# Kernel tuning notes

Measured on AMD Instinct MI355X. Metric: run time of the kernel, lower is better.

## Reference

```python
import jax, jax.numpy as jnp
import numpy as np

EMBED = 1024
HEADS = 16
HEAD_DIM = EMBED // HEADS          # 64
EXP_DIM = 2 * HEAD_DIM             # 128


def setup_inputs() -> dict:
    key = jax.random.key(0)
    ks = jax.random.split(key, 7)
    N, S = 4, 2048
    values = jax.random.normal(ks[0], (N, S, EMBED), dtype=jnp.float32)
    keys_ = jax.random.normal(ks[1], (N, S, EMBED), dtype=jnp.float32)
    query = jax.random.normal(ks[2], (N, S, EMBED), dtype=jnp.float32)
    # feature map linear: initialized to identity weight, zero bias (per init_weights),
    # perturb slightly so it's a nontrivial learned map
    fm_w = jnp.eye(HEAD_DIM, dtype=jnp.float32) + 0.02 * jax.random.normal(ks[3], (HEAD_DIM, HEAD_DIM), dtype=jnp.float32)
    fm_b = 0.02 * jax.random.normal(ks[4], (HEAD_DIM,), dtype=jnp.float32)
    fc_w = jax.random.normal(ks[5], (EMBED, HEADS * EXP_DIM), dtype=jnp.float32) * (1.0 / np.sqrt(HEADS * EXP_DIM))
    fc_b = jnp.zeros((EMBED,), dtype=jnp.float32)
    return {"values": values, "keys": keys_, "query": query,
            "fm_w": fm_w, "fm_b": fm_b, "fc_w": fc_w, "fc_b": fc_b}


def _feature_map(x, fm_w, fm_b):
    # x: [n, s, h, d] -> [n, s, h, 2d]
    z = jnp.einsum('nshd,ed->nshe', x, fm_w) + fm_b
    return jnp.concatenate([jnp.exp(z), jnp.exp(-z)], axis=-1)


def reference(values, keys, query, fm_w, fm_b, fc_w, fc_b):
    N, S, _ = query.shape
    v = values.reshape(N, -1, HEADS, HEAD_DIM)
    k = keys.reshape(N, -1, HEADS, HEAD_DIM)
    q = query.reshape(N, -1, HEADS, HEAD_DIM)
    v, k, q = (_feature_map(x, fm_w, fm_b) for x in (v, k, q))  # [n,s,h,2d]
    scores = jnp.einsum('nqhd,nkhd->nhqk', q, k) / jnp.sqrt(jnp.float32(EMBED))
    attn = jax.nn.softmax(scores, axis=-1)
    out = jnp.einsum('nhql,nlhd->nqhd', attn, v)  # [n,q,h,2d]
    out = out.reshape(N, S, HEADS * EXP_DIM)
    return out @ fc_w.T + fc_b
```

## Files before the change

### kernel.cpp

```cpp
#include <hip/hip_runtime.h>
#include <hip/hip_bf16.h>
#include <stdint.h>

#define N_B 4
#define SEQ 2048
#define NH 16
#define ED 128
#define EMB 1024
#define FCK 2048

typedef float f32x4 __attribute__((ext_vector_type(4)));
typedef float f32x16 __attribute__((ext_vector_type(16)));
typedef _Float16 f16x8 __attribute__((ext_vector_type(8)));
typedef _Float16 f16x4 __attribute__((ext_vector_type(4)));
typedef __fp16 fp16v2 __attribute__((ext_vector_type(2)));

__device__ __forceinline__ void gload16(const void* g, void* l) {
    __builtin_amdgcn_global_load_lds(
        (const __attribute__((address_space(1))) uint32_t*)(g),
        (__attribute__((address_space(3))) uint32_t*)(l), 16, 0, 0);
}

__device__ __forceinline__ int pk2(float a, float b) {
    union { fp16v2 h; int i; } u;
    u.h = __builtin_amdgcn_cvt_pkrtz(a, b);
    return u.i;
}

__device__ __forceinline__ f16x8 frag4(int d0, int d1, int d2, int d3) {
    union { int i[4]; f16x8 v; } u;
    u.i[0] = d0; u.i[1] = d1; u.i[2] = d2; u.i[3] = d3;
    return u.v;
}

__global__ __launch_bounds__(256) void fmap_kernel(
    const float* __restrict__ vals, const float* __restrict__ keys,
    const float* __restrict__ qry,  const float* __restrict__ fmw,
    const float* __restrict__ fmb,
    _Float16* __restrict__ qf, _Float16* __restrict__ kf,
    _Float16* __restrict__ vf)
{
    const int lane = threadIdx.x & 63;
    const int w = threadIdx.x >> 6;
    const int t = blockIdx.x * 4 + w;
    const int n = t >> 11;
    const int s = t & 2047;
    const int r = lane & 15;
    const int g = lane >> 4;

    f16x8 whf[4][2], wlf[4][2];
    #pragma unroll
    for (int te = 0; te < 4; ++te) {
      #pragma unroll
      for (int j = 0; j < 2; ++j) {
        const float* p = fmw + (te*16 + r)*64 + j*32 + 8*g;
        #pragma unroll
        for (int i = 0; i < 8; ++i) {
            float wv = p[i];
            _Float16 hi = (_Float16)wv;
            whf[te][j][i] = hi;
            wlf[te][j][i] = (_Float16)(wv - (float)hi);
        }
      }
    }
    float bias[4];
    #pragma unroll
    for (int te = 0; te < 4; ++te) bias[te] = fmb[te*16 + r];

    const float QSCL = 0.03125f * 1.4426950408889634f;

    const long rowoff = ((long)t*16 + r) * 64;
    const float* srcs[3] = {qry, keys, vals};
    #pragma unroll
    for (int tens = 0; tens < 3; ++tens) {
        const float* src = srcs[tens] + rowoff;
        f16x8 ah[2], al[2];
        #pragma unroll
        for (int j = 0; j < 2; ++j) {
            #pragma unroll
            for (int i = 0; i < 8; ++i) {
                float x = src[j*32 + 8*g + i];
                _Float16 hi = (_Float16)x;
                ah[j][i] = hi;
                al[j][i] = (_Float16)(x - (float)hi);
            }
        }
        #pragma unroll
        for (int te = 0; te < 4; ++te) {
            f32x4 c = (f32x4){0.f,0.f,0.f,0.f};
            c = __builtin_amdgcn_mfma_f32_16x16x32_f16(ah[0], whf[te][0], c, 0, 0, 0);
            c = __builtin_amdgcn_mfma_f32_16x16x32_f16(ah[1], whf[te][1], c, 0, 0, 0);
            c = __builtin_amdgcn_mfma_f32_16x16x32_f16(ah[0], wlf[te][0], c, 0, 0, 0);
            c = __builtin_amdgcn_mfma_f32_16x16x32_f16(ah[1], wlf[te][1], c, 0, 0, 0);
            c = __builtin_amdgcn_mfma_f32_16x16x32_f16(al[0], whf[te][0], c, 0, 0, 0);
            c = __builtin_amdgcn_mfma_f32_16x16x32_f16(al[1], whf[te][1], c, 0, 0, 0);
            #pragma unroll
            for (int i = 0; i < 4; ++i) {
                float z = c[i] + bias[te];
                float ep = __expf(z), en = __expf(-z);
                int hh = 4*g + i;
                int e = te*16 + r;
                long base = (((long)n*NH + hh)*SEQ + s)*ED;
                if (tens == 0) {
                    qf[base + e]      = (_Float16)(ep * QSCL);
                    qf[base + 64 + e] = (_Float16)(en * QSCL);
                } else if (tens == 1) {
                    kf[base + e]      = (_Float16)ep;
                    kf[base + 64 + e] = (_Float16)en;
                } else {
                    vf[base + e]      = (_Float16)ep;
                    vf[base + 64 + e] = (_Float16)en;
                }
            }
        }
    }
}

__global__ __launch_bounds__(256) void vtrans_kernel(
    const _Float16* __restrict__ vf, _Float16* __restrict__ vt)
{
    __shared__ _Float16 tile[64][72];
    const int b = blockIdx.x;
    const int et = b & 1;
    const int st = (b >> 1) & 31;
    const int nh = b >> 6;
    const _Float16* src = vf + ((long)nh*SEQ + st*64)*ED + et*64;
    const int col4 = (threadIdx.x & 15) * 4;
    const int row0 = threadIdx.x >> 4;
    #pragma unroll
    for (int j = 0; j < 4; ++j) {
        int row = row0 + j*16;
        *(f16x4*)&tile[row][col4] = *(const f16x4*)(src + (long)row*ED + col4);
    }
    __syncthreads();
    _Float16* dst = vt + ((long)nh*ED + et*64)*SEQ + st*64;
    const int erow = threadIdx.x >> 2;
    const int sc0 = (threadIdx.x & 3) * 16;
    f16x8 o0, o1;
    #pragma unroll
    for (int i = 0; i < 8; ++i) o0[i] = tile[sc0 + i][erow];
    #pragma unroll
    for (int i = 0; i < 8; ++i) o1[i] = tile[sc0 + 8 + i][erow];
    *(f16x8*)(dst + (long)erow*SEQ + sc0) = o0;
    *(f16x8*)(dst + (long)erow*SEQ + sc0 + 8) = o1;
}

__global__ __launch_bounds__(256) void cvt_kernel(
    const float* __restrict__ src, _Float16* __restrict__ dst)
{
    long i = ((long)blockIdx.x*256 + threadIdx.x)*8;
    f16x8 o;
    #pragma unroll
    for (int j = 0; j < 8; ++j) o[j] = (_Float16)src[i + j];
    *(f16x8*)(dst + i) = o;
}

__global__ __launch_bounds__(512, 2) void attn_kernel(
    const _Float16* __restrict__ qf,
    const _Float16* __restrict__ kf,
    const _Float16* __restrict__ vt,
    _Float16* __restrict__ ob)
{
    __shared__ char smem[65536];
    const int lane = threadIdx.x & 63;
    const int w = threadIdx.x >> 6;
    const int orig = blockIdx.x;
    const int b = ((orig & 7) << 6) | (orig >> 3);
    const int nh = b >> 3;
    const int n = nh >> 4, h = nh & 15;
    const int qt = (b & 7)*8 + w;
    const int q32 = lane & 31;
    const int hl = lane >> 5;

    const _Float16* qb = qf + (long)nh*SEQ*ED;
    const char* kg = (const char*)(kf + (long)nh*SEQ*ED);
    const char* vg = (const char*)(vt + (long)nh*ED*SEQ);

    f16x8 qfr[8];
    #pragma unroll
    for (int j = 0; j < 8; ++j)
        qfr[j] = *(const f16x8*)(qb + (long)(qt*32 + q32)*ED + 16*j + 8*hl);

    auto stage = [&](int kt, int bsel) {
        char* Kl = smem + bsel*32768;
        char* Vl = Kl + 16384;
        const char* kts = kg + (long)kt*64*256;
        const char* vts = vg + (long)kt*64*2;
        #pragma unroll
        for (int i = 0; i < 2; ++i) {
            int row = w*8 + i*4 + (lane>>4);
            int c = (lane&15) ^ (row&15);
            gload16(kts + (long)row*256 + c*16, Kl + (w*8 + i*4)*256);
        }
        #pragma unroll
        for (int i = 0; i < 2; ++i) {
            int row = w*16 + i*8 + (lane>>3);
            int c = (lane&7) ^ (row&7);
            gload16(vts + (long)row*(SEQ*2) + c*16, Vl + (w*16 + i*8)*128);
        }
    };

    f32x16 acc[4];
    #pragma unroll
    for (int vv = 0; vv < 4; ++vv)
      #pragma unroll
      for (int i = 0; i < 16; ++i) acc[vv][i] = 0.f;
    float mrun = -1e30f, lrun = 0.f;

    stage(0, 0);
    __syncthreads();

    const int kswz = q32 & 15;
    const int vswz = q32 & 7;

    for (int kt = 0; kt < SEQ/64; ++kt) {
        const int cur = kt & 1;
        if (kt + 1 < SEQ/64) stage(kt + 1, cur ^ 1);
        const char* Kl = smem + cur*32768;
        const char* Vl = Kl + 16384;

        f32x16 s0, s1;
        #pragma unroll
        for (int i = 0; i < 16; ++i) { s0[i] = 0.f; s1[i] = 0.f; }
        #pragma unroll
        for (int j = 0; j < 8; ++j) {
            int off = (((hl + 2*j) & 15) ^ kswz) << 4;
            f16x8 k0 = *(const f16x8*)(Kl + q32*256 + off);
            f16x8 k1 = *(const f16x8*)(Kl + 8192 + q32*256 + off);
            __builtin_amdgcn_s_setprio(1);
            s0 = __builtin_amdgcn_mfma_f32_32x32x16_f16(k0, qfr[j], s0, 0, 0, 0);
            s1 = __builtin_amdgcn_mfma_f32_32x32x16_f16(k1, qfr[j], s1, 0, 0, 0);
            __builtin_amdgcn_s_setprio(0);
        }

        float mx = s0[0];
        #pragma unroll
        for (int i = 1; i < 16; ++i) mx = fmaxf(mx, s0[i]);
        #pragma unroll
        for (int i = 0; i < 16; ++i) mx = fmaxf(mx, s1[i]);
        mx = fmaxf(mx, __shfl_xor(mx, 32, 64));
        if (__any(mx > mrun + 11.0f)) {
            float mnew = fmaxf(mrun, mx);
            float corr = exp2f(mrun - mnew);
            lrun *= corr;
            #pragma unroll
            for (int vv = 0; vv < 4; ++vv)
                #pragma unroll
                for (int i = 0; i < 16; ++i) acc[vv][i] *= corr;
            mrun = mnew;
        }
        int wreg[2][8];
        float rsum = 0.f;
        #pragma unroll
        for (int kk = 0; kk < 2; ++kk) {
            float p[16];
            #pragma unroll
            for (int i = 0; i < 16; ++i) {
                float sv = (kk == 0) ? s0[i] : s1[i];
                p[i] = exp2f(sv - mrun);
                rsum += p[i];
            }
            #pragma unroll
            for (int tW = 0; tW < 8; ++tW)
                wreg[kk][tW] = pk2(p[2*tW], p[2*tW + 1]);
        }
        rsum += __shfl_xor(rsum, 32, 64);
        lrun += rsum;

        f16x8 pa[4];
        #pragma unroll
        for (int kk = 0; kk < 2; ++kk) {
            #pragma unroll
            for (int par = 0; par < 2; ++par) {
                int a0 = wreg[kk][par*4 + 0], b0 = wreg[kk][par*4 + 2];
                int a1 = wreg[kk][par*4 + 1], b1 = wreg[kk][par*4 + 3];
                auto r0 = __builtin_amdgcn_permlane32_swap(a0, b0, false, false);
                auto r1 = __builtin_amdgcn_permlane32_swap(a1, b1, false, false);
                pa[kk*2 + par] = frag4(r0[0], r1[0], r0[1], r1[1]);
            }
        }

        #pragma unroll
        for (int ks = 0; ks < 4; ++ks) {
            f16x8 vfr[4];
            #pragma unroll
            for (int vv = 0; vv < 4; ++vv) {
                int vrow = vv*32 + q32;
                vfr[vv] = *(const f16x8*)(Vl + vrow*128 + (((2*ks + hl) ^ vswz) << 4));
            }
            __builtin_amdgcn_s_setprio(1);
            #pragma unroll
            for (int vv = 0; vv < 4; ++vv)
                acc[vv] = __builtin_amdgcn_mfma_f32_32x32x16_f16(vfr[vv], pa[ks], acc[vv], 0, 0, 0);
            __builtin_amdgcn_s_setprio(0);
        }
        __syncthreads();
    }

    float inv = 1.0f / lrun;
    int q = qt*32 + q32;
    long base = ((long)n*SEQ + q)*FCK + h*ED;
    #pragma unroll
    for (int vv = 0; vv < 4; ++vv) {
        #pragma unroll
        for (int rg = 0; rg < 4; ++rg) {
            f16x4 o;
            #pragma unroll
            for (int i = 0; i < 4; ++i) o[i] = (_Float16)(acc[vv][rg*4 + i] * inv);
            *(f16x4*)(ob + base + vv*32 + 8*rg + 4*hl) = o;
        }
    }
}

__global__ __launch_bounds__(256) void fc_kernel(
    const _Float16* __restrict__ ob,
    const _Float16* __restrict__ wt,
    const float* __restrict__ fcb,
    float* __restrict__ out)
{
    __shared__ char smem[32768];
    const int lane = threadIdx.x & 63;
    const int w = threadIdx.x >> 6;
    const int wm = w >> 1, wn = w & 1;
    const int r = lane & 15, g = lane >> 4;

    const int orig = blockIdx.x;
    const int tile = ((orig & 7) << 6) | (orig >> 3);
    const int mt = tile >> 3;
    const int nt = tile & 7;

    const char* Ag = (const char*)(ob + (long)mt*128*FCK);
    const char* Bg = (const char*)(wt + (long)nt*128*FCK);

    auto stage = [&](int kt, int bsel) {
        char* As = smem + bsel*16384;
        char* Bs = As + 8192;
        #pragma unroll
        for (int rnd = 0; rnd < 2; ++rnd) {
            int row = rnd*64 + w*16 + (lane >> 2);
            int cs = (lane & 3) ^ ((row >> 1) & 3);
            gload16(Ag + (long)row*(FCK*2) + kt*64 + cs*16, As + rnd*4096 + w*1024);
            gload16(Bg + (long)row*(FCK*2) + kt*64 + cs*16, Bs + rnd*4096 + w*1024);
        }
    };

    f32x4 acc[4][4];
    #pragma unroll
    for (int u = 0; u < 4; ++u)
      #pragma unroll
      for (int v = 0; v < 4; ++v) acc[u][v] = (f32x4){0.f,0.f,0.f,0.f};

    stage(0, 0);
    __syncthreads();

    for (int kt = 0; kt < FCK/32; ++kt) {
        const int cur = kt & 1;
        if (kt + 1 < FCK/32) stage(kt + 1, cur ^ 1);
        const char* As = smem + cur*16384;
        const char* Bs = As + 8192;

        f16x8 afr[4], bfr[4];
        #pragma unroll
        for (int u = 0; u < 4; ++u) {
            int row = wm*64 + u*16 + r;
            afr[u] = *(const f16x8*)(As + row*64 + ((g ^ ((row >> 1) & 3)) << 4));
        }
        #pragma unroll
        for (int v = 0; v < 4; ++v) {
            int row = wn*64 + v*16 + r;
            bfr[v] = *(const f16x8*)(Bs + row*64 + ((g ^ ((row >> 1) & 3)) << 4));
        }
        __builtin_amdgcn_s_setprio(1);
        #pragma unroll
        for (int u = 0; u < 4; ++u)
          #pragma unroll
          for (int v = 0; v < 4; ++v)
            acc[u][v] = __builtin_amdgcn_mfma_f32_16x16x32_f16(afr[u], bfr[v], acc[u][v], 0, 0, 0);
        __builtin_amdgcn_s_setprio(0);
        __syncthreads();
    }

    #pragma unroll
    for (int u = 0; u < 4; ++u)
      #pragma unroll
      for (int v = 0; v < 4; ++v) {
        int col = nt*128 + wn*64 + v*16 + r;
        float bias = fcb[col];
        #pragma unroll
        for (int i = 0; i < 4; ++i) {
            int row = mt*128 + wm*64 + u*16 + 4*g + i;
            out[(long)row*EMB + col] = acc[u][v][i] + bias;
        }
      }
}

extern "C" void kernel_launch(void* const* d_in, const int* in_sizes, int n_in,
                              void* d_out, int out_size, void* d_ws, size_t ws_size,
                              hipStream_t stream) {
    const float* vals = (const float*)d_in[0];
    const float* keys = (const float*)d_in[1];
    const float* qry  = (const float*)d_in[2];
    const float* fmw  = (const float*)d_in[3];
    const float* fmb  = (const float*)d_in[4];
    const float* fcw  = (const float*)d_in[5];
    const float* fcb  = (const float*)d_in[6];
    char* ws = (char*)d_ws;
    const long SZ = 33554432L;
    _Float16* qf = (_Float16*)(ws);
    _Float16* kf = (_Float16*)(ws + SZ);
    _Float16* vf = (_Float16*)(ws + 2*SZ);
    _Float16* vt = (_Float16*)(ws + 3*SZ);
    _Float16* ob = (_Float16*)(ws + 4*SZ);
    _Float16* wt = (_Float16*)(ws + 5*SZ);
    float* out = (float*)d_out;

    fmap_kernel<<<dim3(2048), dim3(256), 0, stream>>>(vals, keys, qry, fmw, fmb, qf, kf, vf);
    vtrans_kernel<<<dim3(4096), dim3(256), 0, stream>>>(vf, vt);
    cvt_kernel<<<dim3(1024), dim3(256), 0, stream>>>(fcw, wt);
    attn_kernel<<<dim3(512), dim3(512), 0, stream>>>(qf, kf, vt, ob);
    fc_kernel<<<dim3(512), dim3(256), 0, stream>>>(ob, wt, fcb, out);
}
```

Before: 297.3 us.

## Double KV tile to 128 keys per stage with 128KB LDS and simplified staging

```diff
diff --git a/kernel.cpp b/kernel.cpp
--- a/kernel.cpp
+++ b/kernel.cpp
@@ -13,6 +13,7 @@
 typedef float f32x16 __attribute__((ext_vector_type(16)));
 typedef _Float16 f16x8 __attribute__((ext_vector_type(8)));
 typedef _Float16 f16x4 __attribute__((ext_vector_type(4)));
+typedef _Float16 f16x2 __attribute__((ext_vector_type(2)));
 typedef __fp16 fp16v2 __attribute__((ext_vector_type(2)));
 
 __device__ __forceinline__ void gload16(const void* g, void* l) {
@@ -27,11 +28,17 @@
     return u.i;
 }
 
+__device__ __forceinline__ f16x2 asf16x2(int v) {
+    union { int i; f16x2 h; } u; u.i = v; return u.h;
+}
+
 __device__ __forceinline__ f16x8 frag4(int d0, int d1, int d2, int d3) {
     union { int i[4]; f16x8 v; } u;
     u.i[0] = d0; u.i[1] = d1; u.i[2] = d2; u.i[3] = d3;
     return u.v;
 }
+
+#define M3(a,b,c) fmaxf(fmaxf((a),(b)),(c))
 
 __global__ __launch_bounds__(256) void fmap_kernel(
     const float* __restrict__ vals, const float* __restrict__ keys,
@@ -161,9 +168,10 @@
     const _Float16* __restrict__ vt,
     _Float16* __restrict__ ob)
 {
-    __shared__ char smem[65536];
-    const int lane = threadIdx.x & 63;
-    const int w = threadIdx.x >> 6;
+    __shared__ char smem[131072];
+    const int tid = threadIdx.x;
+    const int lane = tid & 63;
+    const int w = tid >> 6;
     const int orig = blockIdx.x;
     const int b = ((orig & 7) << 6) | (orig >> 3);
     const int nh = b >> 3;
@@ -181,23 +189,23 @@
     for (int j = 0; j < 8; ++j)
         qfr[j] = *(const f16x8*)(qb + (long)(qt*32 + q32)*ED + 16*j + 8*hl);
 
+    const int srow = tid >> 4;
+    const int sc   = (tid & 15) ^ (srow & 15);
+    const long koff = (long)srow*256  + sc*16;
+    const long voff = (long)srow*4096 + sc*16;
+    const int  ldst = tid*16;
+
     auto stage = [&](int kt, int bsel) {
-        char* Kl = smem + bsel*32768;
-        char* Vl = Kl + 16384;
-        const char* kts = kg + (long)kt*64*256;
-        const char* vts = vg + (long)kt*64*2;
-        #pragma unroll
-        for (int i = 0; i < 2; ++i) {
-            int row = w*8 + i*4 + (lane>>4);
-            int c = (lane&15) ^ (row&15);
-            gload16(kts + (long)row*256 + c*16, Kl + (w*8 + i*4)*256);
-        }
-        #pragma unroll
-        for (int i = 0; i < 2; ++i) {
-            int row = w*16 + i*8 + (lane>>3);
-            int c = (lane&7) ^ (row&7);
-            gload16(vts + (long)row*(SEQ*2) + c*16, Vl + (w*16 + i*8)*128);
-        }
+        char* Kl = smem + bsel*65536;
+        char* Vl = Kl + 32768;
+        const char* ksrc = kg + (long)kt*32768 + koff;
+        const char* vsrc = vg + (long)kt*256   + voff;
+        #pragma unroll
+        for (int i = 0; i < 4; ++i)
+            gload16(ksrc + i*8192, Kl + i*8192 + ldst);
+        #pragma unroll
+        for (int i = 0; i < 4; ++i)
+            gload16(vsrc + (long)i*131072, Vl + i*8192 + ldst);
     };
 
     f32x16 acc[4];
@@ -211,88 +219,95 @@
     __syncthreads();
 
     const int kswz = q32 & 15;
-    const int vswz = q32 & 7;
-
-    for (int kt = 0; kt < SEQ/64; ++kt) {
+
+    for (int kt = 0; kt < SEQ/128; ++kt) {
         const int cur = kt & 1;
-        if (kt + 1 < SEQ/64) stage(kt + 1, cur ^ 1);
-        const char* Kl = smem + cur*32768;
-        const char* Vl = Kl + 16384;
-
-        f32x16 s0, s1;
-        #pragma unroll
-        for (int i = 0; i < 16; ++i) { s0[i] = 0.f; s1[i] = 0.f; }
-        #pragma unroll
-        for (int j = 0; j < 8; ++j) {
-            int off = (((hl + 2*j) & 15) ^ kswz) << 4;
-            f16x8 k0 = *(const f16x8*)(Kl + q32*256 + off);
-            f16x8 k1 = *(const f16x8*)(Kl + 8192 + q32*256 + off);
+        if (kt + 1 < SEQ/128) stage(kt + 1, cur ^ 1);
+        const char* Kl = smem + cur*65536;
+        const char* Vl = Kl + 32768;
+
+        #pragma unroll
+        for (int p = 0; p < 2; ++p) {
+            f32x16 s0, s1;
+            #pragma unroll
+            for (int i = 0; i < 16; ++i) { s0[i] = 0.f; s1[i] = 0.f; }
+            const char* Kb = Kl + (p*64 + q32)*256;
             __builtin_amdgcn_s_setprio(1);
-            s0 = __builtin_amdgcn_mfma_f32_32x32x16_f16(k0, qfr[j], s0, 0, 0, 0);
-            s1 = __builtin_amdgcn_mfma_f32_32x32x16_f16(k1, qfr[j], s1, 0, 0, 0);
+            #pragma unroll
+            for (int j = 0; j < 8; ++j) {
+                int off = (((hl + 2*j) & 15) ^ kswz) << 4;
+                f16x8 k0 = *(const f16x8*)(Kb + off);
+                f16x8 k1 = *(const f16x8*)(Kb + 8192 + off);
+                s0 = __builtin_amdgcn_mfma_f32_32x32x16_f16(k0, qfr[j], s0, 0, 0, 0);
+                s1 = __builtin_amdgcn_mfma_f32_32x32x16_f16(k1, qfr[j], s1, 0, 0, 0);
+            }
             __builtin_amdgcn_s_setprio(0);
-        }
-
-        float mx = s0[0];
-        #pragma unroll
-        for (int i = 1; i < 16; ++i) mx = fmaxf(mx, s0[i]);
-        #pragma unroll
-        for (int i = 0; i < 16; ++i) mx = fmaxf(mx, s1[i]);
-        mx = fmaxf(mx, __shfl_xor(mx, 32, 64));
-        if (__any(mx > mrun + 11.0f)) {
-            float mnew = fmaxf(mrun, mx);
-            float corr = exp2f(mrun - mnew);
-            lrun *= corr;
-            #pragma unroll
-            for (int vv = 0; vv < 4; ++vv)
+
+            float mx = M3(s0[0], s0[1], s0[2]);
+            mx = M3(mx, s0[3], s0[4]);   mx = M3(mx, s0[5], s0[6]);
+            mx = M3(mx, s0[7], s0[8]);   mx = M3(mx, s0[9], s0[10]);
+            mx = M3(mx, s0[11], s0[12]); mx = M3(mx, s0[13], s0[14]);
+            mx = M3(mx, s0[15], s1[0]);  mx = M3(mx, s1[1], s1[2]);
+            mx = M3(mx, s1[3], s1[4]);   mx = M3(mx, s1[5], s1[6]);
+            mx = M3(mx, s1[7], s1[8]);   mx = M3(mx, s1[9], s1[10]);
+            mx = M3(mx, s1[11], s1[12]); mx = M3(mx, s1[13], s1[14]);
+            mx = fmaxf(mx, s1[15]);
+            mx = fmaxf(mx, __shfl_xor(mx, 32, 64));
+            if (__any(mx > mrun + 8.0f)) {
+                float mnew = fmaxf(mrun, mx);
+                float corr = exp2f(mrun - mnew);
+                lrun *= corr;
                 #pragma unroll
-                for (int i = 0; i < 16; ++i) acc[vv][i] *= corr;
-            mrun = mnew;
-        }
-        int wreg[2][8];
-        float rsum = 0.f;
-        #pragma unroll
-        for (int kk = 0; kk < 2; ++kk) {
-            float p[16];
-            #pragma unroll
-            for (int i = 0; i < 16; ++i) {
-                float sv = (kk == 0) ? s0[i] : s1[i];
-                p[i] = exp2f(sv - mrun);
-                rsum += p[i];
-            }
-            #pragma unroll
-            for (int tW = 0; tW < 8; ++tW)
-                wreg[kk][tW] = pk2(p[2*tW], p[2*tW + 1]);
-        }
-        rsum += __shfl_xor(rsum, 32, 64);
-        lrun += rsum;
-
-        f16x8 pa[4];
-        #pragma unroll
-        for (int kk = 0; kk < 2; ++kk) {
-            #pragma unroll
-            for (int par = 0; par < 2; ++par) {
-                int a0 = wreg[kk][par*4 + 0], b0 = wreg[kk][par*4 + 2];
-                int a1 = wreg[kk][par*4 + 1], b1 = wreg[kk][par*4 + 3];
-                auto r0 = __builtin_amdgcn_permlane32_swap(a0, b0, false, false);
-                auto r1 = __builtin_amdgcn_permlane32_swap(a1, b1, false, false);
-                pa[kk*2 + par] = frag4(r0[0], r1[0], r0[1], r1[1]);
-            }
-        }
-
-        #pragma unroll
-        for (int ks = 0; ks < 4; ++ks) {
-            f16x8 vfr[4];
-            #pragma unroll
-            for (int vv = 0; vv < 4; ++vv) {
-                int vrow = vv*32 + q32;
-                vfr[vv] = *(const f16x8*)(Vl + vrow*128 + (((2*ks + hl) ^ vswz) << 4));
-            }
-            __builtin_amdgcn_s_setprio(1);
-            #pragma unroll
-            for (int vv = 0; vv < 4; ++vv)
-                acc[vv] = __builtin_amdgcn_mfma_f32_32x32x16_f16(vfr[vv], pa[ks], acc[vv], 0, 0, 0);
-            __builtin_amdgcn_s_setprio(0);
+                for (int vv = 0; vv < 4; ++vv)
+                    #pragma unroll
+                    for (int i = 0; i < 16; ++i) acc[vv][i] *= corr;
+                mrun = mnew;
+            }
+            int wreg[2][8];
+            f16x2 psum = (f16x2){(_Float16)0.f, (_Float16)0.f};
+            #pragma unroll
+            for (int kk = 0; kk < 2; ++kk) {
+                #pragma unroll
+                for (int tW = 0; tW < 8; ++tW) {
+                    float sa = (kk == 0) ? s0[2*tW]   : s1[2*tW];
+                    float sb = (kk == 0) ? s0[2*tW+1] : s1[2*tW+1];
+                    int pw = pk2(exp2f(sa - mrun), exp2f(sb - mrun));
+                    wreg[kk][tW] = pw;
+                    psum += asf16x2(pw);
+                }
+            }
+            float rsum = (float)psum[0] + (float)psum[1];
+            rsum += __shfl_xor(rsum, 32, 64);
+            lrun += rsum;
+
+            f16x8 pa[4];
+            #pragma unroll
+            for (int kk = 0; kk < 2; ++kk) {
+                #pragma unroll
+                for (int par = 0; par < 2; ++par) {
+                    int a0 = wreg[kk][par*4 + 0], b0 = wreg[kk][par*4 + 2];
+                    int a1 = wreg[kk][par*4 + 1], b1 = wreg[kk][par*4 + 3];
+                    auto r0 = __builtin_amdgcn_permlane32_swap(a0, b0, false, false);
+                    auto r1 = __builtin_amdgcn_permlane32_swap(a1, b1, false, false);
+                    pa[kk*2 + par] = frag4(r0[0], r1[0], r0[1], r1[1]);
+                }
+            }
+
+            #pragma unroll
+            for (int ks = 0; ks < 4; ++ks) {
+                f16x8 vfr[4];
+                #pragma unroll
+                for (int vv = 0; vv < 4; ++vv) {
+                    int vrow = vv*32 + q32;
+                    int c0 = p*8 + ks*2 + hl;
+                    vfr[vv] = *(const f16x8*)(Vl + vrow*256 + ((c0 ^ kswz) << 4));
+                }
+                __builtin_amdgcn_s_setprio(1);
+                #pragma unroll
+                for (int vv = 0; vv < 4; ++vv)
+                    acc[vv] = __builtin_amdgcn_mfma_f32_32x32x16_f16(vfr[vv], pa[ks], acc[vv], 0, 0, 0);
+                __builtin_amdgcn_s_setprio(0);
+            }
         }
         __syncthreads();
     }
```

Measured after the change: 289.4 us. -2.7%, faster.
